# Performance work log

Measured on AMD Instinct MI355X. Metric: run time of the kernel, lower is better.

## Reference

```python
import jax, jax.numpy as jnp
import numpy as np
import math

EPS = 1e-08
KERNEL = 3
PAD = KERNEL // 2


def setup_inputs() -> dict:
    key = jax.random.key(0)
    k1, k2, k3, k4 = jax.random.split(key, 4)
    B, C_in, C_out, H, W, S = 8, 512, 512, 64, 64, 512
    x = jax.random.normal(k1, (B, C_in, H, W), dtype=jnp.float32)
    style = jax.random.normal(k2, (B, S), dtype=jnp.float32)
    # modulation Linear: kaiming_normal fan_in linear => std = 1/sqrt(S); bias filled with 1
    w_mod = jax.random.normal(k3, (C_in, S), dtype=jnp.float32) / math.sqrt(S)
    b_mod = jnp.ones((C_in,), dtype=jnp.float32)
    # conv weight: randn / sqrt(in * k^2)
    weight = jax.random.normal(k4, (1, C_out, C_in, KERNEL, KERNEL), dtype=jnp.float32) / math.sqrt(C_in * KERNEL * KERNEL)
    return {"x": x, "style": style, "w_mod": w_mod, "b_mod": b_mod, "weight": weight}


def _modconv(x, style, w_mod, b_mod, weight):
    # style modulation: (B, S) @ (S, C_in) + bias -> (B, 1, C_in, 1, 1)
    s = style @ w_mod.T + b_mod
    w = weight * s[:, None, :, None, None]            # (B, C_out, C_in, k, k)
    # demodulate: rsqrt of sum of squares over (in, kh, kw)
    demod = jax.lax.rsqrt(jnp.sum(w * w, axis=(2, 3, 4)) + EPS)  # (B, C_out)
    w = w * demod[:, :, None, None, None]

    # groups=B conv == per-sample conv; vmap over batch
    def conv1(xb, wb):
        # xb: (C_in, H, W), wb: (C_out, C_in, k, k)
        return jax.lax.conv_general_dilated(
            xb[None], wb, window_strides=(1, 1),
            padding=[(PAD, PAD), (PAD, PAD)],
            dimension_numbers=("NCHW", "OIHW", "NCHW"))[0]

    return jax.vmap(conv1)(x, w)  # (B, C_out, H, W)


def reference(x, style, w_mod, b_mod, weight):
    return _modconv(x, style, w_mod, b_mod, weight)
```

## Files before the change

kernel.cpp:

```cpp
#include <hip/hip_runtime.h>
#include <hip/hip_bf16.h>

#define BATCH 8
#define CIN   512
#define COUT  512
#define HH    64
#define WW    64
#define SS    512
#define HP    66
#define WP    66
#define NPIX  (HH*WW)

typedef __bf16 bfrag  __attribute__((ext_vector_type(8)));
typedef float  f32x4  __attribute__((ext_vector_type(4)));
typedef unsigned short u16x8 __attribute__((ext_vector_type(8)));

__device__ __forceinline__ void async_copy16(const __hip_bfloat16* g, __hip_bfloat16* l) {
    __builtin_amdgcn_global_load_lds(
        (const __attribute__((address_space(1))) void*)g,
        (__attribute__((address_space(3))) void*)l,
        16, 0, 0);
}

__device__ __forceinline__ bool is_f32(const void* b_mod) {
    return ((const unsigned int*)b_mod)[0] == 0x3F800000u;
}

__global__ void k_prep(const void* __restrict__ style,
                       const void* __restrict__ w_mod,
                       const void* __restrict__ b_mod,
                       const void* __restrict__ weight,
                       float* __restrict__ s_out,
                       float* __restrict__ wsq,
                       __hip_bfloat16* __restrict__ Wt) {
    const bool f32 = is_f32(b_mod);
    if (blockIdx.x < 1024) {
        int tid = blockIdx.x * 256 + threadIdx.x;
        float sq = 0.f;
        if (f32) {
            const float* w = (const float*)weight + (size_t)tid * 9;
#pragma unroll
            for (int k = 0; k < 9; ++k) {
                float v = w[k];
                sq += v * v;
                Wt[k * (COUT * CIN) + tid] = __float2bfloat16(v);
            }
        } else {
            const __hip_bfloat16* w = (const __hip_bfloat16*)weight + (size_t)tid * 9;
#pragma unroll
            for (int k = 0; k < 9; ++k) {
                float v = __bfloat162float(w[k]);
                sq += v * v;
                Wt[k * (COUT * CIN) + tid] = w[k];
            }
        }
        wsq[tid] = sq;
    } else {
        int gw   = (blockIdx.x - 1024) * 4 + (threadIdx.x >> 6);
        int lane = threadIdx.x & 63;
        int b = gw >> 9, i = gw & 511;
        int base = lane * 8;
        float acc = 0.f;
        if (f32) {
            const float* st = (const float*)style + b * SS + base;
            const float* wm = (const float*)w_mod + i * SS + base;
#pragma unroll
            for (int j = 0; j < 8; ++j) acc += st[j] * wm[j];
        } else {
            const __hip_bfloat16* st = (const __hip_bfloat16*)style + b * SS + base;
            const __hip_bfloat16* wm = (const __hip_bfloat16*)w_mod + i * SS + base;
#pragma unroll
            for (int j = 0; j < 8; ++j)
                acc += __bfloat162float(st[j]) * __bfloat162float(wm[j]);
        }
#pragma unroll
        for (int off = 32; off; off >>= 1) acc += __shfl_down(acc, off);
        if (lane == 0) {
            float bias = f32 ? ((const float*)b_mod)[i]
                             : __bfloat162float(((const __hip_bfloat16*)b_mod)[i]);
            s_out[gw] = acc + bias;
        }
    }
}

__global__ void k_mid(const void* __restrict__ xv,
                      const float* __restrict__ s_buf,
                      const float* __restrict__ wsq,
                      const void* __restrict__ b_mod,
                      float* __restrict__ demod,
                      int b0, int nx, int do_demod,
                      __hip_bfloat16* __restrict__ xpad) {
    if ((int)blockIdx.x >= nx) {
        if (!do_demod) return;
        int gw   = ((int)blockIdx.x - nx) * 4 + (threadIdx.x >> 6);
        int lane = threadIdx.x & 63;
        int b = gw >> 9, o = gw & 511;
        int base = lane * 8;
        const float* sp = s_buf + b * CIN + base;
        const float* wp = wsq + o * CIN + base;
        float acc = 0.f;
#pragma unroll
        for (int j = 0; j < 8; ++j) {
            float sv = sp[j];
            acc += sv * sv * wp[j];
        }
#pragma unroll
        for (int off = 32; off; off >>= 1) acc += __shfl_down(acc, off);
        if (lane == 0) demod[gw] = rsqrtf(acc + 1e-8f);
        return;
    }
    const bool f32 = is_f32(b_mod);
    int ic = blockIdx.x & 15;
    int h  = (blockIdx.x >> 4) & 63;
    int bl = blockIdx.x >> 10;
    int b  = b0 + bl;
    int t  = threadIdx.x;
    int g  = t & 3;
    int w  = t >> 2;
    int ch0 = ic * 32 + g * 8;

    float sv[8];
#pragma unroll
    for (int j = 0; j < 8; ++j) sv[j] = s_buf[b * CIN + ch0 + j];

    u16x8 outv;
#pragma unroll
    for (int j = 0; j < 8; ++j) {
        size_t src = (size_t)(b * CIN + ch0 + j) * NPIX + h * WW + w;
        float xval = f32 ? ((const float*)xv)[src]
                         : __bfloat162float(((const __hip_bfloat16*)xv)[src]);
        __hip_bfloat16 bv = __float2bfloat16(xval * sv[j]);
        outv[j] = *(unsigned short*)&bv;
    }
    size_t rowb = (size_t)(bl * HP + h + 1) * WP;
    *(u16x8*)(xpad + (rowb + (w + 1)) * CIN + ch0) = outv;

    u16x8 z = {};
    if (w == 0)  *(u16x8*)(xpad + (rowb + 0)  * CIN + ch0) = z;
    if (w == 63) *(u16x8*)(xpad + (rowb + 65) * CIN + ch0) = z;
    if (h == 0) {
        size_t r0 = (size_t)(bl * HP + 0) * WP;
        *(u16x8*)(xpad + (r0 + (w + 1)) * CIN + ch0) = z;
        if (w == 0)  *(u16x8*)(xpad + (r0 + 0)  * CIN + ch0) = z;
        if (w == 63) *(u16x8*)(xpad + (r0 + 65) * CIN + ch0) = z;
    }
    if (h == 63) {
        size_t r65 = (size_t)(bl * HP + 65) * WP;
        *(u16x8*)(xpad + (r65 + (w + 1)) * CIN + ch0) = z;
        if (w == 0)  *(u16x8*)(xpad + (r65 + 0)  * CIN + ch0) = z;
        if (w == 63) *(u16x8*)(xpad + (r65 + 65) * CIN + ch0) = z;
    }
}

__global__ __launch_bounds__(512, 2)
void k_conv(const __hip_bfloat16* __restrict__ Wt,
            const __hip_bfloat16* __restrict__ xpad,
            const float* __restrict__ demod,
            const void* __restrict__ b_mod, int b0,
            void* __restrict__ outv) {
    __shared__ __hip_bfloat16 sA[2][3][256 * 32];
    __shared__ __hip_bfloat16 sB[2][384 * 32];

    const int tid  = threadIdx.x;
    const int wid  = tid >> 6;
    const int lane = tid & 63;

    const int id     = blockIdx.x;
    const int xcd    = id & 7;
    const int k      = id >> 3;
    const int o_tile = xcd >> 2;
    const int p_tile = (xcd & 3) * 4 + (k & 3);
    const int bl     = k >> 2;
    const int b      = b0 + bl;

    const int o_base = o_tile * 256;
    const int h0     = p_tile * 4;
    const int p_base = p_tile * 256;

    const int sw = ((lane & 3) ^ ((lane >> 3) & 3)) * 8;

    const int arow0 = wid * 32 + (lane >> 2);
    const int arow1 = arow0 + 16;
    const int aoff0 = wid * 1024 + lane * 8;
    const int aoff1 = aoff0 + 512;
    const int asrc0 = (o_base + arow0) * CIN + sw;
    const int asrc1 = (o_base + arow1) * CIN + sw;

    int bdst[3], bsrc[3];
#pragma unroll
    for (int jj = 0; jj < 3; ++jj) {
        int J   = wid * 3 + jj;
        int px  = J * 16 + (lane >> 2);
        int pm  = px < 263 ? px : 263;
        int r   = pm / 66;
        int c   = pm - r * 66;
        bdst[jj] = J * 512 + lane * 8;
        bsrc[jj] = ((bl * HP + h0 + r) * WP + c) * CIN + sw;
    }

    const int quad   = lane >> 4;
    const int l15    = lane & 15;
    const int wave_m = (wid >> 2) * 128;
    const int wave_n = (wid & 3) * 64;
    const int afrag0 = (wave_m + l15) * 32 + ((quad ^ ((l15 >> 1) & 3)) * 8);
    int bfroff[4][3];
#pragma unroll
    for (int nt = 0; nt < 4; ++nt) {
        int n   = wave_n + nt * 16 + l15;
        int pr0 = (n >> 6) * 66 + (n & 63);
#pragma unroll
        for (int kw = 0; kw < 3; ++kw) {
            int pr = pr0 + kw;
            bfroff[nt][kw] = pr * 32 + ((quad ^ ((pr >> 1) & 3)) * 8);
        }
    }

    f32x4 acc[8][4];
#pragma unroll
    for (int mt = 0; mt < 8; ++mt)
#pragma unroll
        for (int nt = 0; nt < 4; ++nt)
            acc[mt][nt] = (f32x4)0.f;

    auto stageB1 = [&](int buf2, int it2, int jj) {
        const int kh = it2 >> 4, i0 = (it2 & 15) << 5;
        async_copy16(xpad + kh * (WP * CIN) + i0 + bsrc[jj], &sB[buf2][bdst[jj]]);
    };
    auto stageA2 = [&](int buf2, int it2, int kw) {
        const int kh = it2 >> 4, i0 = (it2 & 15) << 5;
        const __hip_bfloat16* Ap = Wt + (kh * 3 + kw) * (COUT * CIN) + i0;
        async_copy16(Ap + asrc0, &sA[buf2][kw][aoff0]);
        async_copy16(Ap + asrc1, &sA[buf2][kw][aoff1]);
    };

    bfrag a[8], bb[4];
    auto ldB4 = [&](int buf2, int kw) {
#pragma unroll
        for (int nt = 0; nt < 4; ++nt)
            bb[nt] = *(const bfrag*)(&sB[buf2][bfroff[nt][kw]]);
    };
    auto ldA4 = [&](int buf2, int kw, int mh) {
#pragma unroll
        for (int m = 0; m < 4; ++m)
            a[mh * 4 + m] = *(const bfrag*)(&sA[buf2][kw][afrag0 + (mh * 4 + m) * 512]);
    };
    auto mf16 = [&](int mh) {
        __builtin_amdgcn_s_setprio(1);
#pragma unroll
        for (int m = 0; m < 4; ++m) {
            const int mt = mh * 4 + m;
#pragma unroll
            for (int nt = 0; nt < 4; ++nt)
                acc[mt][nt] = __builtin_amdgcn_mfma_f32_16x16x32_bf16(
                    a[mt], bb[nt], acc[mt][nt], 0, 0, 0);
        }
        __builtin_amdgcn_s_setprio(0);
    };

#define PRE                                                           \
    __builtin_amdgcn_s_barrier();                                     \
    asm volatile("s_waitcnt lgkmcnt(0)" ::: "memory");                \
    __builtin_amdgcn_sched_barrier(0)
#define WAITV(N) asm volatile("s_waitcnt vmcnt(" #N ")" ::: "memory")
#define POST                                                          \
    __builtin_amdgcn_s_barrier();                                     \
    asm volatile("" ::: "memory")

    stageB1(0, 0, 0); stageB1(0, 0, 1); stageB1(0, 0, 2);
    stageA2(0, 0, 0); stageA2(0, 0, 1); stageA2(0, 0, 2);
    WAITV(4);
    POST;

    for (int it = 0; it < 47; ++it) {
        const int buf = it & 1, nb = buf ^ 1, nit = it + 1;
        ldB4(buf, 0); ldA4(buf, 0, 0); stageB1(nb, nit, 0);
        PRE; mf16(0); POST;
        ldA4(buf, 0, 1); stageB1(nb, nit, 1);
        PRE; mf16(1); WAITV(4); POST;
        ldB4(buf, 1); ldA4(buf, 1, 0); stageB1(nb, nit, 2);
        PRE; mf16(0); POST;
        ldA4(buf, 1, 1); stageA2(nb, nit, 0);
        PRE; mf16(1); WAITV(5); POST;
        ldB4(buf, 2); ldA4(buf, 2, 0); stageA2(nb, nit, 1);
        PRE; mf16(0); POST;
        ldA4(buf, 2, 1); stageA2(nb, nit, 2);
        PRE; mf16(1); WAITV(4); POST;
    }
    ldB4(1, 0); ldA4(1, 0, 0);
    PRE; mf16(0); POST;
    ldA4(1, 0, 1);
    PRE; mf16(1); WAITV(2); POST;
    ldB4(1, 1); ldA4(1, 1, 0);
    PRE; mf16(0); POST;
    ldA4(1, 1, 1);
    PRE; mf16(1); WAITV(0); POST;
    ldB4(1, 2); ldA4(1, 2, 0);
    PRE; mf16(0); POST;
    ldA4(1, 2, 1);
    PRE; mf16(1); POST;
#undef PRE
#undef WAITV
#undef POST

    const bool f32 = is_f32(b_mod);
#pragma unroll
    for (int mt = 0; mt < 8; ++mt) {
        const int o0r = o_base + wave_m + mt * 16 + quad * 4;
        float dm[4];
#pragma unroll
        for (int r = 0; r < 4; ++r) dm[r] = demod[b * COUT + o0r + r];
#pragma unroll
        for (int nt = 0; nt < 4; ++nt) {
            const int p = p_base + wave_n + nt * 16 + l15;
#pragma unroll
            for (int r = 0; r < 4; ++r) {
                float val = acc[mt][nt][r] * dm[r];
                size_t idx = (size_t)(b * COUT + o0r + r) * NPIX + p;
                if (f32) ((float*)outv)[idx] = val;
                else     ((__hip_bfloat16*)outv)[idx] = __float2bfloat16(val);
            }
        }
    }
}

extern "C" void kernel_launch(void* const* d_in, const int* in_sizes, int n_in,
                              void* d_out, int out_size, void* d_ws, size_t ws_size,
                              hipStream_t stream) {
    const void* x      = d_in[0];
    const void* style  = d_in[1];
    const void* w_mod  = d_in[2];
    const void* b_mod  = d_in[3];
    const void* weight = d_in[4];

    char* ws = (char*)d_ws;
    float*          s_buf = (float*)(ws + 4096);
    float*          demod = (float*)(ws + 20480);
    float*          wsq   = (float*)(ws + 36864);
    __hip_bfloat16* Wt    = (__hip_bfloat16*)(ws + 1085440);
    __hip_bfloat16* xpad  = (__hip_bfloat16*)(ws + 5804032);

    const size_t need_full = 5804032 + (size_t)BATCH * HP * WP * CIN * 2;
    const int group = (ws_size >= need_full) ? 8 : 4;

    k_prep<<<2048, 256, 0, stream>>>(style, w_mod, b_mod, weight, s_buf, wsq, Wt);

    for (int b0 = 0; b0 < BATCH; b0 += group) {
        const int nx = 1024 * group;
        const int do_demod = (b0 == 0) ? 1 : 0;
        const int nd = do_demod ? 1024 : 0;
        k_mid<<<nx + nd, 256, 0, stream>>>(x, s_buf, wsq, b_mod, demod,
                                           b0, nx, do_demod, xpad);
        k_conv<<<dim3(32 * group), 512, 0, stream>>>(Wt, xpad, demod, b_mod, b0, d_out);
    }
}
```

Baseline: 262.1 us.

## Switch conv GEMM from 16x16x32 to 32x32x16 bf16 MFMA tiles

Replaces the per-wave 8x4 grid of 16x16x32 MFMA tiles with a 4x2 grid of 32x32x16 MFMA tiles, splitting each 32-wide K slice into two 16-deep sub-slices. LDS fragment offsets and the XOR swizzle indexing are recomputed for the 32-lane row layout, and the epilogue is remapped to the 32x32 accumulator layout with vectorized demod loads. The larger MFMA shape needs fewer fragment LDS reads per FLOP and fewer instructions. It changes LDS access patterns, which may cause bank conflicts, and it affects register pressure.

```diff
diff --git a/kernel.cpp b/kernel.cpp
--- a/kernel.cpp
+++ b/kernel.cpp
@@ -13,6 +13,7 @@
 
 typedef __bf16 bfrag  __attribute__((ext_vector_type(8)));
 typedef float  f32x4  __attribute__((ext_vector_type(4)));
+typedef float  f32x16 __attribute__((ext_vector_type(16)));
 typedef unsigned short u16x8 __attribute__((ext_vector_type(8)));
 
 __device__ __forceinline__ void async_copy16(const __hip_bfloat16* g, __hip_bfloat16* l) {
@@ -198,29 +199,38 @@
         bsrc[jj] = ((bl * HP + h0 + r) * WP + c) * CIN + sw;
     }
 
-    const int quad   = lane >> 4;
-    const int l15    = lane & 15;
+    const int l31 = lane & 31;
+    const int q2  = lane >> 5;
     const int wave_m = (wid >> 2) * 128;
     const int wave_n = (wid & 3) * 64;
-    const int afrag0 = (wave_m + l15) * 32 + ((quad ^ ((l15 >> 1) & 3)) * 8);
-    int bfroff[4][3];
-#pragma unroll
-    for (int nt = 0; nt < 4; ++nt) {
-        int n   = wave_n + nt * 16 + l15;
+
+    const int akey  = (l31 >> 1) & 3;
+    const int abase = (wave_m + l31) * 32;
+    int aoffk[2];
+#pragma unroll
+    for (int ksl = 0; ksl < 2; ++ksl)
+        aoffk[ksl] = ((ksl * 2 + q2) ^ akey) * 8;
+
+    int bfro[2][3][2];
+#pragma unroll
+    for (int nt = 0; nt < 2; ++nt) {
+        int n   = wave_n + nt * 32 + l31;
         int pr0 = (n >> 6) * 66 + (n & 63);
 #pragma unroll
         for (int kw = 0; kw < 3; ++kw) {
             int pr = pr0 + kw;
-            bfroff[nt][kw] = pr * 32 + ((quad ^ ((pr >> 1) & 3)) * 8);
-        }
-    }
-
-    f32x4 acc[8][4];
-#pragma unroll
-    for (int mt = 0; mt < 8; ++mt)
-#pragma unroll
-        for (int nt = 0; nt < 4; ++nt)
-            acc[mt][nt] = (f32x4)0.f;
+#pragma unroll
+            for (int ksl = 0; ksl < 2; ++ksl)
+                bfro[nt][kw][ksl] = pr * 32 + (((ksl * 2 + q2) ^ ((pr >> 1) & 3)) * 8);
+        }
+    }
+
+    f32x16 acc[4][2];
+#pragma unroll
+    for (int mt = 0; mt < 4; ++mt)
+#pragma unroll
+        for (int nt = 0; nt < 2; ++nt)
+            acc[mt][nt] = (f32x16)0.f;
 
     auto stageB1 = [&](int buf2, int it2, int jj) {
         const int kh = it2 >> 4, i0 = (it2 & 15) << 5;
@@ -233,27 +243,32 @@
         async_copy16(Ap + asrc1, &sA[buf2][kw][aoff1]);
     };
 
-    bfrag a[8], bb[4];
+    bfrag a2[2][2], bb[2][2];
     auto ldB4 = [&](int buf2, int kw) {
 #pragma unroll
-        for (int nt = 0; nt < 4; ++nt)
-            bb[nt] = *(const bfrag*)(&sB[buf2][bfroff[nt][kw]]);
+        for (int nt = 0; nt < 2; ++nt)
+#pragma unroll
+            for (int ksl = 0; ksl < 2; ++ksl)
+                bb[nt][ksl] = *(const bfrag*)(&sB[buf2][bfro[nt][kw][ksl]]);
     };
     auto ldA4 = [&](int buf2, int kw, int mh) {
 #pragma unroll
-        for (int m = 0; m < 4; ++m)
-            a[mh * 4 + m] = *(const bfrag*)(&sA[buf2][kw][afrag0 + (mh * 4 + m) * 512]);
-    };
-    auto mf16 = [&](int mh) {
+        for (int m = 0; m < 2; ++m)
+#pragma unroll
+            for (int ksl = 0; ksl < 2; ++ksl)
+                a2[m][ksl] = *(const bfrag*)(
+                    &sA[buf2][kw][abase + (mh * 2 + m) * 1024 + aoffk[ksl]]);
+    };
+    auto mf8 = [&](int mh) {
         __builtin_amdgcn_s_setprio(1);
 #pragma unroll
-        for (int m = 0; m < 4; ++m) {
-            const int mt = mh * 4 + m;
-#pragma unroll
-            for (int nt = 0; nt < 4; ++nt)
-                acc[mt][nt] = __builtin_amdgcn_mfma_f32_16x16x32_bf16(
-                    a[mt], bb[nt], acc[mt][nt], 0, 0, 0);
-        }
+        for (int ksl = 0; ksl < 2; ++ksl)
+#pragma unroll
+            for (int m = 0; m < 2; ++m)
+#pragma unroll
+                for (int nt = 0; nt < 2; ++nt)
+                    acc[mh * 2 + m][nt] = __builtin_amdgcn_mfma_f32_32x32x16_bf16(
+                        a2[m][ksl], bb[nt][ksl], acc[mh * 2 + m][nt], 0, 0, 0);
         __builtin_amdgcn_s_setprio(0);
     };
 
@@ -274,50 +289,51 @@
     for (int it = 0; it < 47; ++it) {
         const int buf = it & 1, nb = buf ^ 1, nit = it + 1;
         ldB4(buf, 0); ldA4(buf, 0, 0); stageB1(nb, nit, 0);
-        PRE; mf16(0); POST;
+        PRE; mf8(0); POST;
         ldA4(buf, 0, 1); stageB1(nb, nit, 1);
-        PRE; mf16(1); WAITV(4); POST;
+        PRE; mf8(1); WAITV(4); POST;
         ldB4(buf, 1); ldA4(buf, 1, 0); stageB1(nb, nit, 2);
-        PRE; mf16(0); POST;
+        PRE; mf8(0); POST;
         ldA4(buf, 1, 1); stageA2(nb, nit, 0);
-        PRE; mf16(1); WAITV(5); POST;
+        PRE; mf8(1); WAITV(5); POST;
         ldB4(buf, 2); ldA4(buf, 2, 0); stageA2(nb, nit, 1);
-        PRE; mf16(0); POST;
+        PRE; mf8(0); POST;
         ldA4(buf, 2, 1); stageA2(nb, nit, 2);
-        PRE; mf16(1); WAITV(4); POST;
+        PRE; mf8(1); WAITV(4); POST;
     }
     ldB4(1, 0); ldA4(1, 0, 0);
-    PRE; mf16(0); POST;
+    PRE; mf8(0); POST;
     ldA4(1, 0, 1);
-    PRE; mf16(1); WAITV(2); POST;
+    PRE; mf8(1); WAITV(2); POST;
     ldB4(1, 1); ldA4(1, 1, 0);
-    PRE; mf16(0); POST;
+    PRE; mf8(0); POST;
     ldA4(1, 1, 1);
-    PRE; mf16(1); WAITV(0); POST;
+    PRE; mf8(1); WAITV(0); POST;
     ldB4(1, 2); ldA4(1, 2, 0);
-    PRE; mf16(0); POST;
+    PRE; mf8(0); POST;
     ldA4(1, 2, 1);
-    PRE; mf16(1); POST;
+    PRE; mf8(1); POST;
 #undef PRE
 #undef WAITV
 #undef POST
 
     const bool f32 = is_f32(b_mod);
 #pragma unroll
-    for (int mt = 0; mt < 8; ++mt) {
-        const int o0r = o_base + wave_m + mt * 16 + quad * 4;
-        float dm[4];
-#pragma unroll
-        for (int r = 0; r < 4; ++r) dm[r] = demod[b * COUT + o0r + r];
-#pragma unroll
-        for (int nt = 0; nt < 4; ++nt) {
-            const int p = p_base + wave_n + nt * 16 + l15;
-#pragma unroll
-            for (int r = 0; r < 4; ++r) {
-                float val = acc[mt][nt][r] * dm[r];
-                size_t idx = (size_t)(b * COUT + o0r + r) * NPIX + p;
-                if (f32) ((float*)outv)[idx] = val;
-                else     ((__hip_bfloat16*)outv)[idx] = __float2bfloat16(val);
+    for (int mt = 0; mt < 4; ++mt) {
+#pragma unroll
+        for (int g = 0; g < 4; ++g) {
+            const int orow0 = o_base + wave_m + mt * 32 + g * 8 + 4 * q2;
+            f32x4 dm = *(const f32x4*)(&demod[b * COUT + orow0]);
+#pragma unroll
+            for (int nt = 0; nt < 2; ++nt) {
+                const int p = p_base + wave_n + nt * 32 + l31;
+#pragma unroll
+                for (int j = 0; j < 4; ++j) {
+                    float val = acc[mt][nt][g * 4 + j] * dm[j];
+                    size_t idx = (size_t)(b * COUT + orow0 + j) * NPIX + p;
+                    if (f32) ((float*)outv)[idx] = val;
+                    else     ((__hip_bfloat16*)outv)[idx] = __float2bfloat16(val);
+                }
             }
         }
     }
```

Measured after the change: 275.2 us. 5.0% more time.
